# Kernel tuning notes

Measured on AMD Instinct MI355X. Metric: run time of the kernel, lower is better.

## Reference

```python
import jax, jax.numpy as jnp
import numpy as np

NUM_HEADS = 16


def setup_inputs() -> dict:
    key = jax.random.key(0)
    k1, k2, k3 = jax.random.split(key, 3)
    B, N, C = 4, 2048, 1024
    x = jax.random.normal(k1, (B, N, C), dtype=jnp.float32)
    w_qkv = jax.random.normal(k2, (C, 3 * C), dtype=jnp.float32) * (C ** -0.5)
    w_proj = jax.random.normal(k3, (C, C), dtype=jnp.float32) * (C ** -0.5)
    b_proj = jnp.zeros((C,), dtype=jnp.float32)
    return {"x": x, "w_qkv": w_qkv, "w_proj": w_proj, "b_proj": b_proj}


def reference(x, w_qkv, w_proj, b_proj):
    B, N, C = x.shape
    H = NUM_HEADS
    hd = C // H
    scale = hd ** -0.5
    # qkv projection (no bias), split into q, k, v per head
    qkv = jnp.einsum('bnc,cd->bnd', x, w_qkv)            # [B, N, 3C]
    qkv = qkv.reshape(B, N, 3, H, hd).transpose(0, 3, 2, 1, 4)  # [B, H, 3, N, hd]
    q, k, v = qkv[:, :, 0], qkv[:, :, 1], qkv[:, :, 2]   # each [B, H, N, hd]
    q = q * scale
    attn = jax.nn.softmax(jnp.einsum('bhnd,bhmd->bhnm', q, k), axis=-1)  # [B, H, N, N]
    out = jnp.einsum('bhnm,bhmd->bhnd', attn, v)         # [B, H, N, hd]
    out = out.transpose(0, 2, 1, 3).reshape(B, N, C)
    return jnp.einsum('bnc,cd->bnd', out, w_proj) + b_proj
```

## Files before the change

### kernel.cpp

```cpp
#include <hip/hip_runtime.h>

typedef short s16x8 __attribute__((ext_vector_type(8)));
typedef float f32x4 __attribute__((ext_vector_type(4)));
typedef float f32x16 __attribute__((ext_vector_type(16)));
typedef unsigned u32x4 __attribute__((ext_vector_type(4)));


__device__ __forceinline__ unsigned short bf16bits(float f) {
  unsigned u = __builtin_bit_cast(unsigned, f);
  unsigned rnd = 0x7FFFu + ((u >> 16) & 1u);
  return (unsigned short)((u + rnd) >> 16);
}

__device__ __forceinline__ unsigned pk_bf16(float lo, float hi) {
  unsigned r;
  asm("v_cvt_pk_bf16_f32 %0, %1, %2" : "=v"(r) : "v"(lo), "v"(hi));
  return r;
}

__device__ __forceinline__ void async16(const void* g, void* l) {
  __builtin_amdgcn_global_load_lds((const __attribute__((address_space(1))) void*)g,
                                   (__attribute__((address_space(3))) void*)l, 16, 0, 0);
}

__device__ __forceinline__ f32x4 mfma16(s16x8 a, s16x8 b, f32x4 c) {
  return __builtin_amdgcn_mfma_f32_16x16x32_bf16(a, b, c, 0, 0, 0);
}

__device__ __forceinline__ f32x16 mfma32(s16x8 a, s16x8 b, f32x16 c) {
  return __builtin_amdgcn_mfma_f32_32x32x16_bf16(a, b, c, 0, 0, 0);
}

__device__ __forceinline__ s16x8 lds_frag(const unsigned short* S, int row, int c8, int U) {
  int unit = row * U + (c8 ^ (row & (U - 1)));
  return *(const s16x8*)(S + unit * 8);
}


__global__ __launch_bounds__(256) void cvt_f32_bf16(const float4* __restrict__ in,
                                                    unsigned short* __restrict__ out, int n4) {
  int i = blockIdx.x * blockDim.x + threadIdx.x;
  int stride = gridDim.x * blockDim.x;
  for (; i < n4; i += stride) {
    float4 v = in[i];
    uint2 o;
    o.x = pk_bf16(v.x, v.y);
    o.y = pk_bf16(v.z, v.w);
    *(uint2*)(out + (size_t)i * 4) = o;
  }
}

__global__ __launch_bounds__(256) void transpose_f32_bf16(const float* __restrict__ in,
                                                          unsigned short* __restrict__ out,
                                                          int R, int C) {
  __shared__ float tile[32][33];
  int c0 = blockIdx.x * 32, r0 = blockIdx.y * 32;
  int tx = threadIdx.x, ty = threadIdx.y;
  #pragma unroll
  for (int i = 0; i < 32; i += 8)
    tile[ty + i][tx] = in[(size_t)(r0 + ty + i) * C + c0 + tx];
  __syncthreads();
  #pragma unroll
  for (int i = 0; i < 32; i += 8)
    out[(size_t)(c0 + ty + i) * R + r0 + tx] = bf16bits(tile[tx][ty + i]);
}

__global__ __launch_bounds__(256) void transpose_v(const unsigned short* __restrict__ V,
                                                   unsigned short* __restrict__ Vt) {
  __shared__ unsigned short sm[64 * 68];
  int bh = blockIdx.y, kt0 = blockIdx.x * 64;
  const unsigned short* v = V + (size_t)bh * 2048 * 64 + (size_t)kt0 * 64;
  unsigned short* vt = Vt + (size_t)bh * 64 * 2048;
  int t = threadIdx.x;
  #pragma unroll
  for (int i = 0; i < 4; ++i) {
    int u = i * 256 + t;
    int f = u * 4;
    int k = f >> 6, d0 = f & 63;
    *(uint2*)&sm[k * 68 + d0] = *(const uint2*)&v[f];
  }
  __syncthreads();
  #pragma unroll
  for (int j = 0; j < 16; ++j) {
    int o = j * 256 + t;
    int d = o >> 6, k = o & 63;
    vt[(size_t)d * 2048 + kt0 + k] = sm[k * 68 + d];
  }
}


template <typename EPI>
__global__ __launch_bounds__(256) void gemm_bt(const unsigned short* __restrict__ A,
                                               const unsigned short* __restrict__ Bt,
                                               int K, EPI epi) {
  __shared__ __align__(16) unsigned short As[128 * 64];
  __shared__ __align__(16) unsigned short Bs[128 * 64];
  const int tid = threadIdx.x, wid = tid >> 6, lane = tid & 63;
  const int quad = lane >> 4, l16 = lane & 15;
  const int bm0 = blockIdx.y * 128, bn0 = blockIdx.x * 128;
  const int wm = (wid & 1) * 64, wn = (wid >> 1) * 64;
  f32x4 acc[4][4] = {};

  for (int kt = 0; kt < K; kt += 64) {
    #pragma unroll
    for (int t = 0; t < 4; ++t) {
      int c = wid * 4 + t;
      int u = c * 64 + lane;
      int row = u >> 3;
      int c8 = (u & 7) ^ (row & 7);
      async16(A + (size_t)(bm0 + row) * K + kt + c8 * 8, (char*)As + c * 1024);
      async16(Bt + (size_t)(bn0 + row) * K + kt + c8 * 8, (char*)Bs + c * 1024);
    }
    __syncthreads();
    #pragma unroll
    for (int kk = 0; kk < 2; ++kk) {
      s16x8 a[4], b[4];
      #pragma unroll
      for (int i = 0; i < 4; ++i) a[i] = lds_frag(As, wm + i * 16 + l16, kk * 4 + quad, 8);
      #pragma unroll
      for (int j = 0; j < 4; ++j) b[j] = lds_frag(Bs, wn + j * 16 + l16, kk * 4 + quad, 8);
      #pragma unroll
      for (int i = 0; i < 4; ++i)
        #pragma unroll
        for (int j = 0; j < 4; ++j)
          acc[i][j] = mfma16(a[i], b[j], acc[i][j]);
    }
    __syncthreads();
  }
  #pragma unroll
  for (int i = 0; i < 4; ++i)
    #pragma unroll
    for (int j = 0; j < 4; ++j)
      epi.store4(bm0 + wm + i * 16 + quad * 4, bn0 + wn + j * 16 + l16, acc[i][j]);
}

struct QKVEpi {
  unsigned short *Q, *K, *V;
  float qscale;
  __device__ __forceinline__ void store4(int m0, int n, f32x4 v) const {
    int s = m0 >> 10, h = (m0 >> 6) & 15, d = m0 & 63;
    int b = n >> 11, ns = n & 2047;
    unsigned short* dst = (s == 0) ? Q : ((s == 1) ? K : V);
    float sc = (s == 0) ? qscale : 1.f;
    uint2 o;
    o.x = pk_bf16(v[0] * sc, v[1] * sc);
    o.y = pk_bf16(v[2] * sc, v[3] * sc);
    *(uint2*)&dst[(((size_t)b * 16 + h) * 2048 + ns) * 64 + d] = o;
  }
};

struct ProjEpi {
  const float* bias;
  float* out;
  __device__ __forceinline__ void store4(int m0, int n, f32x4 v) const {
    float4 b4 = *(const float4*)&bias[m0];
    float4 o = {v[0] + b4.x, v[1] + b4.y, v[2] + b4.z, v[3] + b4.w};
    *(float4*)&out[(size_t)n * 1024 + m0] = o;
  }
};

__global__ __launch_bounds__(256, 3) void flash_attn(const unsigned short* __restrict__ Q,
                                                     const unsigned short* __restrict__ K,
                                                     const unsigned short* __restrict__ Vt,
                                                     unsigned short* __restrict__ O) {
  __shared__ __align__(16) unsigned short Ks[2][64 * 64];
  __shared__ __align__(16) unsigned short Vs[2][64 * 64];
  const int tid = threadIdx.x, wid = tid >> 6, lane = tid & 63;
  const int l31 = lane & 31, half = lane >> 5;
  const int bh = blockIdx.y, qt = blockIdx.x;
  const unsigned short* Qg = Q + (size_t)bh * 2048 * 64;
  const unsigned short* Kg = K + (size_t)bh * 2048 * 64;
  const unsigned short* Vg = Vt + (size_t)bh * 64 * 2048;
  const int q0 = qt * 256 + wid * 64;

  s16x8 qB[2][4];
  #pragma unroll
  for (int g = 0; g < 2; ++g) {
    int qrow = q0 + g * 32 + l31;
    #pragma unroll
    for (int s = 0; s < 4; ++s)
      qB[g][s] = *(const s16x8*)&Qg[(size_t)qrow * 64 + s * 16 + half * 8];
  }

  const int c0 = wid * 2, c1 = wid * 2 + 1;
  const int u0 = c0 * 64 + lane, u1 = c1 * 64 + lane;
  const int kr0 = u0 >> 3, kc0 = ((u0 & 7) ^ (kr0 & 7)) * 8;
  const int kr1 = u1 >> 3, kc1 = ((u1 & 7) ^ (kr1 & 7)) * 8;

  auto stage = [&](int kt, int buf) {
    const int kb = kt * 64;
    async16(Kg + (size_t)(kb + kr0) * 64 + kc0, (char*)&Ks[buf][0] + c0 * 1024);
    async16(Kg + (size_t)(kb + kr1) * 64 + kc1, (char*)&Ks[buf][0] + c1 * 1024);
    async16(Vg + (size_t)kr0 * 2048 + kb + kc0, (char*)&Vs[buf][0] + c0 * 1024);
    async16(Vg + (size_t)kr1 * 2048 + kb + kc1, (char*)&Vs[buf][0] + c1 * 1024);
  };

  f32x16 oacc[2][2] = {};
  float l_i[2] = {0.f, 0.f};
  const f32x16 fz = {};

  stage(0, 0);
  for (int kt = 0; kt < 32; ++kt) {
    const int cur = kt & 1;
    __syncthreads();
    if (kt + 1 < 32) stage(kt + 1, cur ^ 1);
    const unsigned short* ks = &Ks[cur][0];
    const unsigned short* vs = &Vs[cur][0];

    #pragma unroll
    for (int kf = 0; kf < 2; ++kf) {
      f32x16 st[2];
      {
        s16x8 a = lds_frag(ks, kf * 32 + l31, half, 8);
        st[0] = mfma32(a, qB[0][0], fz);
        st[1] = mfma32(a, qB[1][0], fz);
      }
      #pragma unroll
      for (int s = 1; s < 4; ++s) {
        s16x8 a = lds_frag(ks, kf * 32 + l31, s * 2 + half, 8);
        st[0] = mfma32(a, qB[0][s], st[0]);
        st[1] = mfma32(a, qB[1][s], st[1]);
      }
      #pragma unroll
      for (int g = 0; g < 2; ++g) {
        float rs = 0.f;
        #pragma unroll
        for (int r = 0; r < 16; ++r) {
          float p = __builtin_amdgcn_exp2f(st[g][r]);
          st[g][r] = p;
          rs += p;
        }
        rs += __shfl_xor(rs, 32);
        l_i[g] += rs;
      }
      #pragma unroll
      for (int t = 0; t < 2; ++t) {
        int rb = t * 8;
        u32x4 bP[2];
        #pragma unroll
        for (int g = 0; g < 2; ++g) {
          unsigned pa0 = pk_bf16(st[g][rb + 0], st[g][rb + 1]);
          unsigned pa1 = pk_bf16(st[g][rb + 2], st[g][rb + 3]);
          unsigned pb0 = pk_bf16(st[g][rb + 4], st[g][rb + 5]);
          unsigned pb1 = pk_bf16(st[g][rb + 6], st[g][rb + 7]);
          unsigned s0 = half ? pa0 : pb0;
          unsigned s1 = half ? pa1 : pb1;
          unsigned r0 = (unsigned)__shfl_xor((int)s0, 32);
          unsigned r1 = (unsigned)__shfl_xor((int)s1, 32);
          bP[g][0] = half ? r0 : pa0;
          bP[g][1] = half ? r1 : pa1;
          bP[g][2] = half ? pb0 : r0;
          bP[g][3] = half ? pb1 : r1;
        }
        #pragma unroll
        for (int f = 0; f < 2; ++f) {
          s16x8 aV = lds_frag(vs, f * 32 + l31, (kf * 2 + t) * 2 + half, 8);
          oacc[0][f] = mfma32(aV, __builtin_bit_cast(s16x8, bP[0]), oacc[0][f]);
          oacc[1][f] = mfma32(aV, __builtin_bit_cast(s16x8, bP[1]), oacc[1][f]);
        }
      }
    }
  }

  const int b = bh >> 4, h = bh & 15;
  #pragma unroll
  for (int g = 0; g < 2; ++g) {
    float inv = 1.f / l_i[g];
    int qrow = q0 + g * 32 + l31;
    size_t base = (((size_t)b * 2048 + qrow) * 16 + h) * 64;
    #pragma unroll
    for (int f = 0; f < 2; ++f)
      #pragma unroll
      for (int q = 0; q < 4; ++q) {
        int d0 = f * 32 + q * 8 + half * 4;
        uint2 o;
        o.x = pk_bf16(oacc[g][f][q * 4 + 0] * inv, oacc[g][f][q * 4 + 1] * inv);
        o.y = pk_bf16(oacc[g][f][q * 4 + 2] * inv, oacc[g][f][q * 4 + 3] * inv);
        *(uint2*)&O[base + d0] = o;
      }
  }
}


extern "C" void kernel_launch(void* const* d_in, const int* in_sizes, int n_in,
                              void* d_out, int out_size, void* d_ws, size_t ws_size,
                              hipStream_t stream) {
  (void)in_sizes; (void)n_in; (void)out_size; (void)ws_size;
  const float* x = (const float*)d_in[0];
  const float* w_qkv = (const float*)d_in[1];
  const float* w_proj = (const float*)d_in[2];
  const float* b_proj = (const float*)d_in[3];
  float* out = (float*)d_out;
  char* ws = (char*)d_ws;
  const size_t MB = 1ull << 20;
  unsigned short* Xb  = (unsigned short*)(ws);
  unsigned short* Wqt = (unsigned short*)(ws + 16 * MB);
  unsigned short* Wpt = (unsigned short*)(ws + 22 * MB);
  unsigned short* Qb  = (unsigned short*)(ws + 24 * MB);
  unsigned short* Kb  = (unsigned short*)(ws + 40 * MB);
  unsigned short* Vb  = (unsigned short*)(ws + 56 * MB);
  unsigned short* Vt  = Xb;
  unsigned short* Ob  = Vb;

  cvt_f32_bf16<<<2048, 256, 0, stream>>>((const float4*)x, Xb, 8388608 / 4);
  transpose_f32_bf16<<<dim3(96, 32), dim3(32, 8), 0, stream>>>(w_qkv, Wqt, 1024, 3072);
  transpose_f32_bf16<<<dim3(32, 32), dim3(32, 8), 0, stream>>>(w_proj, Wpt, 1024, 1024);

  QKVEpi e1{Qb, Kb, Vb, 0.125f * 1.44269504088896340736f};
  gemm_bt<QKVEpi><<<dim3(64, 24), 256, 0, stream>>>(Wqt, Xb, 1024, e1);

  transpose_v<<<dim3(32, 64), 256, 0, stream>>>(Vb, Vt);
  flash_attn<<<dim3(8, 64), 256, 0, stream>>>(Qb, Kb, Vt, Ob);

  ProjEpi e2{b_proj, out};
  gemm_bt<ProjEpi><<<dim3(64, 8), 256, 0, stream>>>(Wpt, Ob, 1024, e2);
}
```

Measured before the change: 284.6 us.

## Halve per-warp query rows, store K/V tiles in fragment order in LDS

Each warp now handles 32 query rows instead of 64, so each block covers 128 queries and the grid doubles to 16x64 blocks. Launch bounds rise to 4 blocks per CU. K and V tiles are staged into LDS already laid out in MFMA fragment order, with two warps loading K and two loading V, so fragment reads become simple contiguous 16-byte loads without swizzle math. The exp row sum is split into four partial accumulators to shorten the dependency chain. This lowers register pressure and raises occupancy, but halves reuse of each K/V tile per block, so K/V traffic from L2 doubles.

```diff
diff --git a/kernel.cpp b/kernel.cpp
--- a/kernel.cpp
+++ b/kernel.cpp
@@ -159,44 +159,46 @@
   }
 };
 
-__global__ __launch_bounds__(256, 3) void flash_attn(const unsigned short* __restrict__ Q,
+__global__ __launch_bounds__(256, 4) void flash_attn(const unsigned short* __restrict__ Q,
                                                      const unsigned short* __restrict__ K,
                                                      const unsigned short* __restrict__ Vt,
                                                      unsigned short* __restrict__ O) {
-  __shared__ __align__(16) unsigned short Ks[2][64 * 64];
-  __shared__ __align__(16) unsigned short Vs[2][64 * 64];
+  __shared__ __align__(16) unsigned short Ks[2][8 * 512];
+  __shared__ __align__(16) unsigned short Vs[2][8 * 512];
   const int tid = threadIdx.x, wid = tid >> 6, lane = tid & 63;
   const int l31 = lane & 31, half = lane >> 5;
   const int bh = blockIdx.y, qt = blockIdx.x;
   const unsigned short* Qg = Q + (size_t)bh * 2048 * 64;
   const unsigned short* Kg = K + (size_t)bh * 2048 * 64;
   const unsigned short* Vg = Vt + (size_t)bh * 64 * 2048;
-  const int q0 = qt * 256 + wid * 64;
-
-  s16x8 qB[2][4];
-  #pragma unroll
-  for (int g = 0; g < 2; ++g) {
-    int qrow = q0 + g * 32 + l31;
-    #pragma unroll
-    for (int s = 0; s < 4; ++s)
-      qB[g][s] = *(const s16x8*)&Qg[(size_t)qrow * 64 + s * 16 + half * 8];
-  }
-
-  const int c0 = wid * 2, c1 = wid * 2 + 1;
-  const int u0 = c0 * 64 + lane, u1 = c1 * 64 + lane;
-  const int kr0 = u0 >> 3, kc0 = ((u0 & 7) ^ (kr0 & 7)) * 8;
-  const int kr1 = u1 >> 3, kc1 = ((u1 & 7) ^ (kr1 & 7)) * 8;
+  const int qrow = qt * 128 + wid * 32 + l31;
+
+  s16x8 qB[4];
+  #pragma unroll
+  for (int s = 0; s < 4; ++s)
+    qB[s] = *(const s16x8*)&Qg[(size_t)qrow * 64 + s * 16 + half * 8];
+
+  const bool isK = wid < 2;
+  int sA[4];
+  #pragma unroll
+  for (int t = 0; t < 4; ++t) {
+    int c = (wid & 1) * 4 + t;
+    if (isK) sA[t] = ((c >> 2) * 32 + l31) * 64 + ((c & 3) * 2 + half) * 8;
+    else     sA[t] = ((c & 1) * 32 + l31) * 2048 + (c >> 1) * 16 + half * 8;
+  }
 
   auto stage = [&](int kt, int buf) {
     const int kb = kt * 64;
-    async16(Kg + (size_t)(kb + kr0) * 64 + kc0, (char*)&Ks[buf][0] + c0 * 1024);
-    async16(Kg + (size_t)(kb + kr1) * 64 + kc1, (char*)&Ks[buf][0] + c1 * 1024);
-    async16(Vg + (size_t)kr0 * 2048 + kb + kc0, (char*)&Vs[buf][0] + c0 * 1024);
-    async16(Vg + (size_t)kr1 * 2048 + kb + kc1, (char*)&Vs[buf][0] + c1 * 1024);
+    #pragma unroll
+    for (int t = 0; t < 4; ++t) {
+      int c = (wid & 1) * 4 + t;
+      if (isK) async16(Kg + (size_t)kb * 64 + sA[t], (char*)&Ks[buf][0] + c * 1024);
+      else     async16(Vg + kb + sA[t],              (char*)&Vs[buf][0] + c * 1024);
+    }
   };
 
-  f32x16 oacc[2][2] = {};
-  float l_i[2] = {0.f, 0.f};
+  f32x16 oacc[2] = {};
+  float l_i = 0.f;
   const f32x16 fz = {};
 
   stage(0, 0);
@@ -209,76 +211,67 @@
 
     #pragma unroll
     for (int kf = 0; kf < 2; ++kf) {
-      f32x16 st[2];
+      f32x16 st;
       {
-        s16x8 a = lds_frag(ks, kf * 32 + l31, half, 8);
-        st[0] = mfma32(a, qB[0][0], fz);
-        st[1] = mfma32(a, qB[1][0], fz);
+        s16x8 a = *(const s16x8*)&ks[((kf * 4 + 0) * 64 + lane) * 8];
+        st = mfma32(a, qB[0], fz);
       }
       #pragma unroll
       for (int s = 1; s < 4; ++s) {
-        s16x8 a = lds_frag(ks, kf * 32 + l31, s * 2 + half, 8);
-        st[0] = mfma32(a, qB[0][s], st[0]);
-        st[1] = mfma32(a, qB[1][s], st[1]);
+        s16x8 a = *(const s16x8*)&ks[((kf * 4 + s) * 64 + lane) * 8];
+        st = mfma32(a, qB[s], st);
       }
-      #pragma unroll
-      for (int g = 0; g < 2; ++g) {
-        float rs = 0.f;
-        #pragma unroll
-        for (int r = 0; r < 16; ++r) {
-          float p = __builtin_amdgcn_exp2f(st[g][r]);
-          st[g][r] = p;
-          rs += p;
-        }
-        rs += __shfl_xor(rs, 32);
-        l_i[g] += rs;
+      float a0 = 0.f, a1 = 0.f, a2 = 0.f, a3 = 0.f;
+      #pragma unroll
+      for (int r = 0; r < 16; r += 4) {
+        float p0 = __builtin_amdgcn_exp2f(st[r + 0]);
+        float p1 = __builtin_amdgcn_exp2f(st[r + 1]);
+        float p2 = __builtin_amdgcn_exp2f(st[r + 2]);
+        float p3 = __builtin_amdgcn_exp2f(st[r + 3]);
+        st[r + 0] = p0; st[r + 1] = p1; st[r + 2] = p2; st[r + 3] = p3;
+        a0 += p0; a1 += p1; a2 += p2; a3 += p3;
       }
+      float rs = (a0 + a1) + (a2 + a3);
+      rs += __shfl_xor(rs, 32);
+      l_i += rs;
       #pragma unroll
       for (int t = 0; t < 2; ++t) {
         int rb = t * 8;
-        u32x4 bP[2];
-        #pragma unroll
-        for (int g = 0; g < 2; ++g) {
-          unsigned pa0 = pk_bf16(st[g][rb + 0], st[g][rb + 1]);
-          unsigned pa1 = pk_bf16(st[g][rb + 2], st[g][rb + 3]);
-          unsigned pb0 = pk_bf16(st[g][rb + 4], st[g][rb + 5]);
-          unsigned pb1 = pk_bf16(st[g][rb + 6], st[g][rb + 7]);
-          unsigned s0 = half ? pa0 : pb0;
-          unsigned s1 = half ? pa1 : pb1;
-          unsigned r0 = (unsigned)__shfl_xor((int)s0, 32);
-          unsigned r1 = (unsigned)__shfl_xor((int)s1, 32);
-          bP[g][0] = half ? r0 : pa0;
-          bP[g][1] = half ? r1 : pa1;
-          bP[g][2] = half ? pb0 : r0;
-          bP[g][3] = half ? pb1 : r1;
-        }
+        unsigned pa0 = pk_bf16(st[rb + 0], st[rb + 1]);
+        unsigned pa1 = pk_bf16(st[rb + 2], st[rb + 3]);
+        unsigned pb0 = pk_bf16(st[rb + 4], st[rb + 5]);
+        unsigned pb1 = pk_bf16(st[rb + 6], st[rb + 7]);
+        unsigned s0 = half ? pa0 : pb0;
+        unsigned s1 = half ? pa1 : pb1;
+        unsigned r0 = (unsigned)__shfl_xor((int)s0, 32);
+        unsigned r1 = (unsigned)__shfl_xor((int)s1, 32);
+        u32x4 bP;
+        bP[0] = half ? r0 : pa0;
+        bP[1] = half ? r1 : pa1;
+        bP[2] = half ? pb0 : r0;
+        bP[3] = half ? pb1 : r1;
         #pragma unroll
         for (int f = 0; f < 2; ++f) {
-          s16x8 aV = lds_frag(vs, f * 32 + l31, (kf * 2 + t) * 2 + half, 8);
-          oacc[0][f] = mfma32(aV, __builtin_bit_cast(s16x8, bP[0]), oacc[0][f]);
-          oacc[1][f] = mfma32(aV, __builtin_bit_cast(s16x8, bP[1]), oacc[1][f]);
+          s16x8 aV = *(const s16x8*)&vs[(((kf * 2 + t) * 2 + f) * 64 + lane) * 8];
+          oacc[f] = mfma32(aV, __builtin_bit_cast(s16x8, bP), oacc[f]);
         }
       }
     }
   }
 
   const int b = bh >> 4, h = bh & 15;
-  #pragma unroll
-  for (int g = 0; g < 2; ++g) {
-    float inv = 1.f / l_i[g];
-    int qrow = q0 + g * 32 + l31;
-    size_t base = (((size_t)b * 2048 + qrow) * 16 + h) * 64;
-    #pragma unroll
-    for (int f = 0; f < 2; ++f)
-      #pragma unroll
-      for (int q = 0; q < 4; ++q) {
-        int d0 = f * 32 + q * 8 + half * 4;
-        uint2 o;
-        o.x = pk_bf16(oacc[g][f][q * 4 + 0] * inv, oacc[g][f][q * 4 + 1] * inv);
-        o.y = pk_bf16(oacc[g][f][q * 4 + 2] * inv, oacc[g][f][q * 4 + 3] * inv);
-        *(uint2*)&O[base + d0] = o;
-      }
-  }
+  float inv = 1.f / l_i;
+  size_t base = (((size_t)b * 2048 + qrow) * 16 + h) * 64;
+  #pragma unroll
+  for (int f = 0; f < 2; ++f)
+    #pragma unroll
+    for (int q = 0; q < 4; ++q) {
+      int d0 = f * 32 + q * 8 + half * 4;
+      uint2 o;
+      o.x = pk_bf16(oacc[f][q * 4 + 0] * inv, oacc[f][q * 4 + 1] * inv);
+      o.y = pk_bf16(oacc[f][q * 4 + 2] * inv, oacc[f][q * 4 + 3] * inv);
+      *(uint2*)&O[base + d0] = o;
+    }
 }
 
 
@@ -310,7 +303,7 @@
   gemm_bt<QKVEpi><<<dim3(64, 24), 256, 0, stream>>>(Wqt, Xb, 1024, e1);
 
   transpose_v<<<dim3(32, 64), 256, 0, stream>>>(Vb, Vt);
-  flash_attn<<<dim3(8, 64), 256, 0, stream>>>(Qb, Kb, Vt, Ob);
+  flash_attn<<<dim3(16, 64), 256, 0, stream>>>(Qb, Kb, Vt, Ob);
 
   ProjEpi e2{b_proj, out};
   gemm_bt<ProjEpi><<<dim3(64, 8), 256, 0, stream>>>(Wpt, Ob, 1024, e2);
```

Result: slower. 296.6 us (+4.2%).
